# Optimization experiments

Hardware: AMD Instinct MI355X
Metric: run time of the kernel (lower is better)

Reference implementation:

```python
import jax, jax.numpy as jnp
import numpy as np

G, B, T, H = 14, 64, 2048, 6  # nb_gaussians, batch, track_len, nb_hidden_variables
LOG_2PI = float(np.log(2.0 * np.pi))


def _dnn(x, d):
    # tf.math.divide_no_nan, safe under autodiff
    d_safe = jnp.where(d == 0, 1.0, d)
    return jnp.where(d == 0, 0.0, x / d_safe)


def _norm_log_gaussian(t):
    return -0.5 * (LOG_2PI + t ** 2)


def _gaussian_product(c1, c2, n1, n2, b1, b2, k):
    # RNN_gaussian_product: combine gaussians 1,2 so output-3 no longer depends
    # on coef k and output-4 carries it. (Tiny 1e-20/1e-100 TF noise terms are
    # numerically void and omitted.)
    C1 = c1[:, :, k:k + 1]  # [B,T,1]
    C2 = c2[:, :, k:k + 1]
    cc1, cc2 = _dnn(c1, C1), _dnn(c2, C2)
    nn1, nn2 = _dnn(n1, C1), _dnn(n2, C2)
    bb1, bb2 = _dnn(b1, C1[:, :, 0]), _dnn(b2, C2[:, :, 0])
    var1 = 1.0 / C1 ** 2
    var2 = 1.0 / C2 ** 2
    var3 = var1 + var2
    std3 = jnp.sqrt(var3)
    c3 = (cc1 - cc2) / std3
    n3 = (nn1 - nn2) / std3
    b3 = (bb1 - bb2) / std3[:, :, 0]
    var4 = var1 * var2 / var3
    std4 = jnp.sqrt(var4)
    den = var3 * std4
    c4 = (cc1 * var2 + cc2 * var1) / den
    n4 = (nn1 * var2 + nn2 * var1) / den
    b4 = (bb1 * var2[:, :, 0] + bb2 * var1[:, :, 0]) / den[:, :, 0]
    logC = -jnp.log(jnp.abs(C1 * C2 * std4 * std3))[:, :, 0]
    return logC, c3, c4, n3, n4, b3, b4


def _forward(cur, nxt, biases):
    nH = cur.shape[-1]
    cur_l = list(cur)
    nxt_l = list(nxt)
    b_l = list(biases)
    LC = jnp.zeros(cur.shape[1:3], cur.dtype)  # [B,T]
    # Phase 1: integrate out each current hidden variable k.
    for k in range(nH):
        n = len(b_l)
        for i in range(n - 1):
            logC, c3, c4, n3, n4, b3, b4 = _gaussian_product(
                cur_l[i], cur_l[i + 1], nxt_l[i], nxt_l[i + 1], b_l[i], b_l[i + 1], k)
            cur_l[i], cur_l[i + 1] = c3, c4
            nxt_l[i], nxt_l[i + 1] = n3, n4
            b_l[i], b_l[i + 1] = b3, b4
            LC = LC + logC
        # final_RNN_function_phase_1: integrate & drop last dependent gaussian
        LC = LC - jnp.log(jnp.abs(cur_l[n - 1][:, :, k]))
        cur_l.pop(n - 1)
        nxt_l.pop(n - 1)
        b_l.pop(n - 1)
    # Phase 2: roles of current/next swapped; pop dependent gaussian into kept.
    kept_n, kept_b = [], []
    for k in range(nH):
        n = len(b_l)
        for i in range(n - 1):
            logC, n3, n4, c3, c4, b3, b4 = _gaussian_product(
                nxt_l[i], nxt_l[i + 1], cur_l[i], cur_l[i + 1], b_l[i], b_l[i + 1], k)
            nxt_l[i], nxt_l[i + 1] = n3, n4
            cur_l[i], cur_l[i + 1] = c3, c4
            b_l[i], b_l[i + 1] = b3, b4
            LC = LC + logC
        kept_n.append(nxt_l.pop(n - 1))
        kept_b.append(b_l.pop(n - 1))
        cur_l.pop(n - 1)
    # Remaining gaussians are pure constants
    LC = LC + jnp.sum(_norm_log_gaussian(jnp.stack(b_l)), axis=0)
    return jnp.stack(kept_n), jnp.stack(kept_b), LC


def setup_inputs() -> dict:
    key = jax.random.key(0)
    ks = jax.random.split(key, 5)

    def coefs(k1, k2, shape):
        mag = jax.random.uniform(k1, shape, jnp.float32, 0.5, 1.5)
        sgn = jnp.where(jax.random.bernoulli(k2, 0.5, shape), 1.0, -1.0)
        return mag * sgn

    cur = coefs(ks[0], ks[1], (G, B, T, H))
    nxt = coefs(ks[2], ks[3], (G, B, T, H))
    biases = jax.random.normal(ks[4], (G, B, T), jnp.float32)
    return {"current_hidden_var_coefs": cur,
            "next_hidden_var_coefs": nxt,
            "biases": biases}


def reference(current_hidden_var_coefs, next_hidden_var_coefs, biases):
    return _forward(current_hidden_var_coefs, next_hidden_var_coefs, biases)
```

## Files before the change

kernel.cpp:

```cpp
#include <hip/hip_runtime.h>

#define Gc 14
#define Hc 6
#define NPc (64*2048)
#define LOG_2PI 1.8378770664093453f

typedef float v2f __attribute__((ext_vector_type(2)));

__device__ __forceinline__ float frsq(float x){ return __builtin_amdgcn_rsqf(x); }

template<int CTRL>
__device__ __forceinline__ float dppf(float x){
    union { float f; int i; } u; u.f = x;
    u.i = __builtin_amdgcn_update_dpp(0, u.i, CTRL, 0xF, 0xF, true);
    return u.f;
}
template<int OQ>
__device__ __forceinline__ float bcast(float x){
    return (OQ == 0) ? dppf<0xA0>(x) : dppf<0xF5>(x);
}

template<int J, int C, int N, int OQ>
__device__ __forceinline__ void sweep(v2f (&st)[Gc][3], float (&bb)[Gc]){
#pragma unroll
    for (int i = 0; i < N - 1; ++i){
        const float C1 = bcast<OQ>(st[i][J][C]);
        const float C2 = bcast<OQ>(st[i + 1][J][C]);
        const float S  = frsq(fmaf(C1, C1, C2 * C2));
        const float s1 = C2 * S, s2 = C1 * S;
        const float a1 = copysignf(s1, C1), a2 = copysignf(s2, C2);
        const v2f A1 = {a1, a1}, A2 = {a2, a2}, S1 = {s1, s1}, S2 = {s2, s2};
#pragma unroll
        for (int j = 0; j < 3; ++j){
            const v2f x = st[i][j], y = st[i + 1][j];
            const v2f t = y * A2, u = y * S1;
            st[i][j]     = __builtin_elementwise_fma(x, A1, -t);
            st[i + 1][j] = __builtin_elementwise_fma(x, S2, u);
        }
        {
            const float x = bb[i], y = bb[i + 1];
            bb[i]     = fmaf(x, a1, -(y * a2));
            bb[i + 1] = fmaf(x, s2, y * s1);
        }
    }
}

__global__ void __launch_bounds__(256, 2)
gaussmerge_kernel(const float* __restrict__ cur_in,
                  const float* __restrict__ nxt_in,
                  const float* __restrict__ b_in,
                  float* __restrict__ out)
{
    const int tid = threadIdx.x;
    const int q = tid & 1;
    const int p = blockIdx.x * 128 + (tid >> 1);

    v2f   st[Gc][3];
    float bb[Gc];

    const float* abase = (q ? nxt_in : cur_in) + (size_t)p * Hc;
    const float* bp    = b_in + p;
#pragma unroll
    for (int g = 0; g < Gc; ++g){
        const v2f* a = (const v2f*)(abase + (size_t)g * (NPc * Hc));
        st[g][0] = a[0]; st[g][1] = a[1]; st[g][2] = a[2];
        bb[g] = bp[(size_t)g * NPc];
    }

    float LC = 0.0f;

    sweep<0, 0, 14, 0>(st, bb); LC -= __logf(fabsf(st[13][0][0]));
    sweep<0, 1, 13, 0>(st, bb); LC -= __logf(fabsf(st[12][0][1]));
    sweep<1, 0, 12, 0>(st, bb); LC -= __logf(fabsf(st[11][1][0]));
    sweep<1, 1, 11, 0>(st, bb); LC -= __logf(fabsf(st[10][1][1]));
    sweep<2, 0, 10, 0>(st, bb); LC -= __logf(fabsf(st[ 9][2][0]));
    sweep<2, 1,  9, 0>(st, bb); LC -= __logf(fabsf(st[ 8][2][1]));

    float* outN = out;
    float* outB = out + (size_t)Hc * NPc * Hc;
    float* outL = outB + (size_t)Hc * NPc;

#define PH2(K, J, C, N)                                                         \
    sweep<J, C, N, 1>(st, bb);                                                  \
    {                                                                           \
        constexpr int m = 7 - (K);                                              \
        if (q) {                                                                \
            v2f* o = (v2f*)(outN + (size_t)(K) * (NPc * Hc) + (size_t)p * Hc);  \
            o[0] = st[m][0]; o[1] = st[m][1]; o[2] = st[m][2];                  \
        } else {                                                                \
            outB[(size_t)(K) * NPc + p] = bb[m];                                \
        }                                                                       \
    }

    PH2(0, 0, 0, 8)
    PH2(1, 0, 1, 7)
    PH2(2, 1, 0, 6)
    PH2(3, 1, 1, 5)
    PH2(4, 2, 0, 4)
    PH2(5, 2, 1, 3)
#undef PH2

    LC += -0.5f * (LOG_2PI + bb[0] * bb[0]);
    LC += -0.5f * (LOG_2PI + bb[1] * bb[1]);
    if (q == 0) outL[p] = LC;
}

extern "C" void kernel_launch(void* const* d_in, const int* in_sizes, int n_in,
                              void* d_out, int out_size, void* d_ws, size_t ws_size,
                              hipStream_t stream) {
    const float* cur = (const float*)d_in[0];
    const float* nxt = (const float*)d_in[1];
    const float* bia = (const float*)d_in[2];
    float* out = (float*)d_out;

    dim3 grid((NPc * 2) / 256), block(256);
    gaussmerge_kernel<<<grid, block, 0, stream>>>(cur, nxt, bia, out);
}
```

Measured before the change: 31.25 us.

## Skew Givens sweeps into a wavefront tick schedule for cross-sweep ILP

Replaces the sequential per-variable elimination sweeps with a compile-time wavefront schedule. Sweep K now starts two steps after sweep K-1, so independent rotations from different sweeps are interleaved within each tick. Phase 2 sweeps are overlapped with the tail of phase 1 in the same way. The aim is to expose instruction-level parallelism and hide the latency of the rsq and DPP broadcast dependency chains, at the cost of more template machinery and possibly higher register pressure or longer live ranges.

Measured after the change: 31.30 us. About the same (+0.2%).

```diff
diff --git a/kernel.cpp b/kernel.cpp
--- a/kernel.cpp
+++ b/kernel.cpp
@@ -1,4 +1,5 @@
 #include <hip/hip_runtime.h>
+#include <utility>
 
 #define Gc 14
 #define Hc 6
@@ -20,29 +21,71 @@
     return (OQ == 0) ? dppf<0xA0>(x) : dppf<0xF5>(x);
 }
 
-template<int J, int C, int N, int OQ>
-__device__ __forceinline__ void sweep(v2f (&st)[Gc][3], float (&bb)[Gc]){
+template<int J, int C, int OQ, int I>
+__device__ __forceinline__ void gstep(v2f (&st)[Gc][3], float (&bb)[Gc]){
+    const float C1 = bcast<OQ>(st[I][J][C]);
+    const float C2 = bcast<OQ>(st[I+1][J][C]);
+    const float S  = frsq(fmaf(C1, C1, C2 * C2));
+    const float s1 = C2 * S, s2 = C1 * S;
+    const float a1 = copysignf(s1, C1), a2 = copysignf(s2, C2);
+    const v2f A1 = {a1, a1}, A2 = {a2, a2}, S1 = {s1, s1}, S2 = {s2, s2};
 #pragma unroll
-    for (int i = 0; i < N - 1; ++i){
-        const float C1 = bcast<OQ>(st[i][J][C]);
-        const float C2 = bcast<OQ>(st[i + 1][J][C]);
-        const float S  = frsq(fmaf(C1, C1, C2 * C2));
-        const float s1 = C2 * S, s2 = C1 * S;
-        const float a1 = copysignf(s1, C1), a2 = copysignf(s2, C2);
-        const v2f A1 = {a1, a1}, A2 = {a2, a2}, S1 = {s1, s1}, S2 = {s2, s2};
-#pragma unroll
-        for (int j = 0; j < 3; ++j){
-            const v2f x = st[i][j], y = st[i + 1][j];
-            const v2f t = y * A2, u = y * S1;
-            st[i][j]     = __builtin_elementwise_fma(x, A1, -t);
-            st[i + 1][j] = __builtin_elementwise_fma(x, S2, u);
-        }
-        {
-            const float x = bb[i], y = bb[i + 1];
-            bb[i]     = fmaf(x, a1, -(y * a2));
-            bb[i + 1] = fmaf(x, s2, y * s1);
+    for (int j = 0; j < 3; ++j){
+        const v2f x = st[I][j], y = st[I+1][j];
+        st[I][j]     = __builtin_elementwise_fma(x, A1, -(y * A2));
+        st[I + 1][j] = __builtin_elementwise_fma(x, S2, y * S1);
+    }
+    const float x = bb[I], y = bb[I + 1];
+    bb[I]     = fmaf(x, a1, -(y * a2));
+    bb[I + 1] = fmaf(x, s2, y * s1);
+}
+
+template<int T, int K>
+__device__ __forceinline__ void p1_at(v2f (&st)[Gc][3], float (&bb)[Gc], float &LC){
+    constexpr int i = T - 2 * K;
+    constexpr int n = Gc - K;
+    if constexpr (i >= 0 && i <= n - 2)
+        gstep<(K >> 1), (K & 1), 0, (i & 31)>(st, bb);
+    if constexpr (i == n - 1)
+        LC -= __logf(fabsf(st[n - 1][K >> 1][K & 1]));
+}
+
+template<int T, int K>
+__device__ __forceinline__ void p2_at(v2f (&st)[Gc][3], float (&bb)[Gc],
+                                      float* __restrict__ outN, float* __restrict__ outB,
+                                      int p, int q){
+    constexpr int i = T - 12 - 2 * K;
+    constexpr int n = (Gc - Hc) - K;
+    if constexpr (i >= 0 && i <= n - 2)
+        gstep<(K >> 1), (K & 1), 1, (i & 31)>(st, bb);
+    if constexpr (i == n - 1){
+        constexpr int m = n - 1;
+        if (q){
+            v2f* o = (v2f*)(outN + (size_t)K * (NPc * Hc) + (size_t)p * Hc);
+            o[0] = st[m][0]; o[1] = st[m][1]; o[2] = st[m][2];
+        } else {
+            outB[(size_t)K * NPc + p] = bb[m];
         }
     }
+}
+
+template<int T>
+__device__ __forceinline__ void tick(v2f (&st)[Gc][3], float (&bb)[Gc], float &LC,
+                                     float* __restrict__ outN, float* __restrict__ outB,
+                                     int p, int q){
+    p1_at<T, 0>(st, bb, LC); p1_at<T, 1>(st, bb, LC); p1_at<T, 2>(st, bb, LC);
+    p1_at<T, 3>(st, bb, LC); p1_at<T, 4>(st, bb, LC); p1_at<T, 5>(st, bb, LC);
+    p2_at<T, 0>(st, bb, outN, outB, p, q); p2_at<T, 1>(st, bb, outN, outB, p, q);
+    p2_at<T, 2>(st, bb, outN, outB, p, q); p2_at<T, 3>(st, bb, outN, outB, p, q);
+    p2_at<T, 4>(st, bb, outN, outB, p, q); p2_at<T, 5>(st, bb, outN, outB, p, q);
+}
+
+template<int... Ts>
+__device__ __forceinline__ void run_ticks(std::integer_sequence<int, Ts...>,
+                                          v2f (&st)[Gc][3], float (&bb)[Gc], float &LC,
+                                          float* __restrict__ outN, float* __restrict__ outB,
+                                          int p, int q){
+    (tick<Ts>(st, bb, LC, outN, outB, p, q), ...);
 }
 
 __global__ void __launch_bounds__(256, 2)
@@ -69,36 +112,11 @@
 
     float LC = 0.0f;
 
-    sweep<0, 0, 14, 0>(st, bb); LC -= __logf(fabsf(st[13][0][0]));
-    sweep<0, 1, 13, 0>(st, bb); LC -= __logf(fabsf(st[12][0][1]));
-    sweep<1, 0, 12, 0>(st, bb); LC -= __logf(fabsf(st[11][1][0]));
-    sweep<1, 1, 11, 0>(st, bb); LC -= __logf(fabsf(st[10][1][1]));
-    sweep<2, 0, 10, 0>(st, bb); LC -= __logf(fabsf(st[ 9][2][0]));
-    sweep<2, 1,  9, 0>(st, bb); LC -= __logf(fabsf(st[ 8][2][1]));
-
     float* outN = out;
     float* outB = out + (size_t)Hc * NPc * Hc;
     float* outL = outB + (size_t)Hc * NPc;
 
-#define PH2(K, J, C, N)                                                         \
-    sweep<J, C, N, 1>(st, bb);                                                  \
-    {                                                                           \
-        constexpr int m = 7 - (K);                                              \
-        if (q) {                                                                \
-            v2f* o = (v2f*)(outN + (size_t)(K) * (NPc * Hc) + (size_t)p * Hc);  \
-            o[0] = st[m][0]; o[1] = st[m][1]; o[2] = st[m][2];                  \
-        } else {                                                                \
-            outB[(size_t)(K) * NPc + p] = bb[m];                                \
-        }                                                                       \
-    }
-
-    PH2(0, 0, 0, 8)
-    PH2(1, 0, 1, 7)
-    PH2(2, 1, 0, 6)
-    PH2(3, 1, 1, 5)
-    PH2(4, 2, 0, 4)
-    PH2(5, 2, 1, 3)
-#undef PH2
+    run_ticks(std::make_integer_sequence<int, 25>{}, st, bb, LC, outN, outB, p, q);
 
     LC += -0.5f * (LOG_2PI + bb[0] * bb[0]);
     LC += -0.5f * (LOG_2PI + bb[1] * bb[1]);
```

## Stream gaussians through a systolic rotation pipeline with prefetch instead of full-register sweeps

Applied to the files above, without the earlier changes.

The kernel used to load all 14 gaussians into registers and then run 12 triangular sweeps over them. It now streams one gaussian per loop iteration through six phase-1 and six phase-2 stages. Each stage keeps only a single accumulator state, and the next gaussian's loads are prefetched while the current one is processed. This cuts live register state, which should allow more occupancy, and overlaps global loads with compute. In exchange the stage guards run inside a non-unrolled loop with runtime g checks, which may add branch and select overhead. The rotation order also changes, with the accumulator kept in the bottom slot, so numerical equivalence depends on the reformulated order matching the original.

Result: slower. 97.97 us (+213.6%).

```diff
diff --git a/kernel.cpp b/kernel.cpp
--- a/kernel.cpp
+++ b/kernel.cpp
@@ -20,29 +20,58 @@
     return (OQ == 0) ? dppf<0xA0>(x) : dppf<0xF5>(x);
 }
 
-template<int J, int C, int N, int OQ>
-__device__ __forceinline__ void sweep(v2f (&st)[Gc][3], float (&bb)[Gc]){
+
+struct Coef { float a1, a2, s1, s2; };
+
+template<int OQ, int J, int C>
+__device__ __forceinline__ Coef mkcoef(const v2f* cv, const v2f* rv){
+    const float C1 = bcast<OQ>(cv[J][C]);
+    const float C2 = bcast<OQ>(rv[J][C]);
+    const float S  = frsq(fmaf(C1, C1, C2 * C2));
+    Coef c;
+    c.s1 = C2 * S; c.s2 = C1 * S;
+    c.a1 = copysignf(c.s1, C1);
+    c.a2 = copysignf(c.s2, C2);
+    return c;
+}
+
+__device__ __forceinline__ void rot3(v2f* cv, v2f (&rv)[3], const Coef& c){
+    const v2f A1 = {c.a1, c.a1}, A2 = {c.a2, c.a2}, S1 = {c.s1, c.s1}, S2 = {c.s2, c.s2};
 #pragma unroll
-    for (int i = 0; i < N - 1; ++i){
-        const float C1 = bcast<OQ>(st[i][J][C]);
-        const float C2 = bcast<OQ>(st[i + 1][J][C]);
-        const float S  = frsq(fmaf(C1, C1, C2 * C2));
-        const float s1 = C2 * S, s2 = C1 * S;
-        const float a1 = copysignf(s1, C1), a2 = copysignf(s2, C2);
-        const v2f A1 = {a1, a1}, A2 = {a2, a2}, S1 = {s1, s1}, S2 = {s2, s2};
-#pragma unroll
-        for (int j = 0; j < 3; ++j){
-            const v2f x = st[i][j], y = st[i + 1][j];
-            const v2f t = y * A2, u = y * S1;
-            st[i][j]     = __builtin_elementwise_fma(x, A1, -t);
-            st[i + 1][j] = __builtin_elementwise_fma(x, S2, u);
-        }
-        {
-            const float x = bb[i], y = bb[i + 1];
-            bb[i]     = fmaf(x, a1, -(y * a2));
-            bb[i + 1] = fmaf(x, s2, y * s1);
-        }
+    for (int j = 0; j < 3; ++j){
+        const v2f x = cv[j], y = rv[j];
+        rv[j] = __builtin_elementwise_fma(x, A1, -(y * A2));
+        cv[j] = __builtin_elementwise_fma(x, S2, y * S1);
     }
+}
+
+struct St1 { v2f v[3]; float b; };
+struct St2 { v2f v[3]; };
+
+template<int K>
+__device__ __forceinline__ void stage_p1(int g, St1& s, v2f (&r)[3], float& rb){
+    if (g < K) return;
+    if (g == K){
+        s.v[0] = r[0]; s.v[1] = r[1]; s.v[2] = r[2]; s.b = rb;
+        return;
+    }
+    const Coef c = mkcoef<0, (K >> 1), (K & 1)>(s.v, r);
+    rot3(s.v, r, c);
+    const float x = s.b, y = rb;
+    rb  = fmaf(x, c.a1, -(y * c.a2));
+    s.b = fmaf(x, c.s2,   y * c.s1);
+}
+
+template<int K>
+__device__ __forceinline__ void stage_p2(int g, St2& s, v2f (&r)[3]){
+    constexpr int START = 6 + K;
+    if (g < START) return;
+    if (g == START){
+        s.v[0] = r[0]; s.v[1] = r[1]; s.v[2] = r[2];
+        return;
+    }
+    const Coef c = mkcoef<1, (K >> 1), (K & 1)>(s.v, r);
+    rot3(s.v, r, c);
 }
 
 __global__ void __launch_bounds__(256, 2)
@@ -55,53 +84,67 @@
     const int q = tid & 1;
     const int p = blockIdx.x * 128 + (tid >> 1);
 
-    v2f   st[Gc][3];
-    float bb[Gc];
-
     const float* abase = (q ? nxt_in : cur_in) + (size_t)p * Hc;
     const float* bp    = b_in + p;
-#pragma unroll
+
+    St1 s1[6];
+    St2 s2[6];
+    float LC = 0.0f;
+
+    v2f nr[3]; float nrb;
+    { const v2f* a = (const v2f*)abase; nr[0] = a[0]; nr[1] = a[1]; nr[2] = a[2]; nrb = bp[0]; }
+
+#pragma unroll 1
     for (int g = 0; g < Gc; ++g){
-        const v2f* a = (const v2f*)(abase + (size_t)g * (NPc * Hc));
-        st[g][0] = a[0]; st[g][1] = a[1]; st[g][2] = a[2];
-        bb[g] = bp[(size_t)g * NPc];
+        v2f r[3] = {nr[0], nr[1], nr[2]};
+        float rb = nrb;
+        if (g + 1 < Gc){
+            const v2f* a = (const v2f*)(abase + (size_t)(g + 1) * (NPc * Hc));
+            nr[0] = a[0]; nr[1] = a[1]; nr[2] = a[2];
+            nrb = bp[(size_t)(g + 1) * NPc];
+        }
+
+        stage_p1<0>(g, s1[0], r, rb);
+        stage_p1<1>(g, s1[1], r, rb);
+        stage_p1<2>(g, s1[2], r, rb);
+        stage_p1<3>(g, s1[3], r, rb);
+        stage_p1<4>(g, s1[4], r, rb);
+        stage_p1<5>(g, s1[5], r, rb);
+
+        if (g >= 6 && q == 0) r[0] = (v2f){rb, 0.0f};
+
+        stage_p2<0>(g, s2[0], r);
+        stage_p2<1>(g, s2[1], r);
+        stage_p2<2>(g, s2[2], r);
+        stage_p2<3>(g, s2[3], r);
+        stage_p2<4>(g, s2[4], r);
+        stage_p2<5>(g, s2[5], r);
+
+        if (g >= 12){
+            const float bd = r[0].x;
+            LC += -0.5f * (LOG_2PI + bd * bd);
+        }
     }
 
-    float LC = 0.0f;
-
-    sweep<0, 0, 14, 0>(st, bb); LC -= __logf(fabsf(st[13][0][0]));
-    sweep<0, 1, 13, 0>(st, bb); LC -= __logf(fabsf(st[12][0][1]));
-    sweep<1, 0, 12, 0>(st, bb); LC -= __logf(fabsf(st[11][1][0]));
-    sweep<1, 1, 11, 0>(st, bb); LC -= __logf(fabsf(st[10][1][1]));
-    sweep<2, 0, 10, 0>(st, bb); LC -= __logf(fabsf(st[ 9][2][0]));
-    sweep<2, 1,  9, 0>(st, bb); LC -= __logf(fabsf(st[ 8][2][1]));
+    LC -= __logf(fabsf(s1[0].v[0].x));
+    LC -= __logf(fabsf(s1[1].v[0].y));
+    LC -= __logf(fabsf(s1[2].v[1].x));
+    LC -= __logf(fabsf(s1[3].v[1].y));
+    LC -= __logf(fabsf(s1[4].v[2].x));
+    LC -= __logf(fabsf(s1[5].v[2].y));
 
     float* outN = out;
     float* outB = out + (size_t)Hc * NPc * Hc;
     float* outL = outB + (size_t)Hc * NPc;
-
-#define PH2(K, J, C, N)                                                         \
-    sweep<J, C, N, 1>(st, bb);                                                  \
-    {                                                                           \
-        constexpr int m = 7 - (K);                                              \
-        if (q) {                                                                \
-            v2f* o = (v2f*)(outN + (size_t)(K) * (NPc * Hc) + (size_t)p * Hc);  \
-            o[0] = st[m][0]; o[1] = st[m][1]; o[2] = st[m][2];                  \
-        } else {                                                                \
-            outB[(size_t)(K) * NPc + p] = bb[m];                                \
-        }                                                                       \
+#pragma unroll
+    for (int k = 0; k < 6; ++k){
+        if (q){
+            v2f* o = (v2f*)(outN + (size_t)k * (NPc * Hc) + (size_t)p * Hc);
+            o[0] = s2[k].v[0]; o[1] = s2[k].v[1]; o[2] = s2[k].v[2];
+        } else {
+            outB[(size_t)k * NPc + p] = s2[k].v[0].x;
+        }
     }
-
-    PH2(0, 0, 0, 8)
-    PH2(1, 0, 1, 7)
-    PH2(2, 1, 0, 6)
-    PH2(3, 1, 1, 5)
-    PH2(4, 2, 0, 4)
-    PH2(5, 2, 1, 3)
-#undef PH2
-
-    LC += -0.5f * (LOG_2PI + bb[0] * bb[0]);
-    LC += -0.5f * (LOG_2PI + bb[1] * bb[1]);
     if (q == 0) outL[p] = LC;
 }
 
```
